# Optimization experiments

Measured on AMD Instinct MI355X. Metric: run time of the kernel, lower is better.

The kernel has to match this reference:

```python
import jax, jax.numpy as jnp
import numpy as np

B, T, C = 2, 2048, 1024
HS = 64              # head_size
H = C // HS          # 16 heads
DW, DA, DV, DG = 64, 64, 32, 160   # RWKV-7 LoRA dims for C=1024
FFN = 4 * C
GN_EPS = 64e-5       # ln_x GroupNorm eps from source


def _layernorm(h, w, b, eps=1e-5):
    mu = jnp.mean(h, axis=-1, keepdims=True)
    var = jnp.mean(jnp.square(h - mu), axis=-1, keepdims=True)
    return (h - mu) * jax.lax.rsqrt(var + eps) * w + b


def _time_shift_delta(h):
    # ZeroPad2d((0,0,1,-1))(h) - h : previous-token delta
    return jnp.pad(h, ((0, 0), (1, 0), (0, 0)))[:, :-1, :] - h


def _wkv7_scan(decay, r, k, v, a, b, S0):
    # all inputs [B,T,H,N]; state S [B,H,N_v,N_k]
    # S_t = S_{t-1} * diag(decay_t) + (S_{t-1} @ a_t) b_t^T + v_t k_t^T ; y_t = S_t @ r_t
    def step(S, inp):
        w_t, r_t, k_t, v_t, a_t, b_t = inp
        S = S * w_t[:, :, None, :]
        sa = jnp.einsum('bhij,bhj->bhi', S, a_t)
        S = S + sa[..., None] * b_t[:, :, None, :] + v_t[..., None] * k_t[:, :, None, :]
        y = jnp.einsum('bhij,bhj->bhi', S, r_t)
        return S, y
    seq = tuple(jnp.moveaxis(t, 1, 0) for t in (decay, r, k, v, a, b))
    S_last, y = jax.lax.scan(step, S0, seq)
    return jnp.moveaxis(y, 0, 1), S_last


def _block_forward(x, v_first, init_state, ln1_w, ln1_b, ln2_w, ln2_b,
                   x_r, x_w, x_k, x_v, x_a, x_g, w0, w1, w2, a0, a1, a2,
                   v0, v1, v2, g1, g2, k_k, k_a, r_k, W_r, W_k, W_v, W_o,
                   ln_x_w, ln_x_b, mix_k_ffn, W_key_ffn, W_val_ffn):
    # ---- time-mix (RWKV_Tmix_x070), layer_idx = 1 ----
    xn = _layernorm(x, ln1_w, ln1_b)
    xx = _time_shift_delta(xn)
    xr = xn + xx * x_r
    xw = xn + xx * x_w
    xk = xn + xx * x_k
    xv = xn + xx * x_v
    xa = xn + xx * x_a
    xg = xn + xx * x_g
    r = xr @ W_r.T
    w = -jax.nn.softplus(-(w0 + jnp.tanh(xw @ w1) @ w2)) - 0.5   # w <= -0.5
    k = xk @ W_k.T
    v = xv @ W_v.T
    v = v + (v_first - v) * jax.nn.sigmoid(v0 + (xv @ v1) @ v2)  # layer_idx > 0 path
    a = jax.nn.sigmoid(a0 + (xa @ a1) @ a2)
    g = jax.nn.sigmoid(xg @ g1) @ g2
    kk = (k * k_k).reshape(B, T, H, HS)
    kk = kk / jnp.maximum(jnp.linalg.norm(kk, axis=-1, keepdims=True), 1e-12)
    k = k * (1.0 + (a - 1.0) * k_a)
    r4 = r.reshape(B, T, H, HS)
    k4 = k.reshape(B, T, H, HS)
    v4 = v.reshape(B, T, H, HS)
    a4 = a.reshape(B, T, H, HS)
    decay = jnp.exp(w).reshape(B, T, H, HS)
    y, S_last = _wkv7_scan(decay, r4, k4, v4, -kk, kk * a4, init_state)
    # GroupNorm(H groups, eps=64e-5) over C, per (b,t)
    mu = jnp.mean(y, axis=-1, keepdims=True)
    var = jnp.mean(jnp.square(y - mu), axis=-1, keepdims=True)
    y = ((y - mu) * jax.lax.rsqrt(var + GN_EPS)).reshape(B, T, C) * ln_x_w + ln_x_b
    y = y + (jnp.sum(r4 * k4 * r_k, axis=-1, keepdims=True) * v4).reshape(B, T, C)
    x = x + (y * g) @ W_o.T
    # ---- channel-mix (RWKV_CMix_x070) ----
    xn2 = _layernorm(x, ln2_w, ln2_b)
    kf = xn2 + _time_shift_delta(xn2) * mix_k_ffn
    kf = jnp.square(jax.nn.relu(kf @ W_key_ffn.T))
    x = x + kf @ W_val_ffn.T
    return x, v_first


def setup_inputs():
    key = jax.random.key(0)
    ks = iter(jax.random.split(key, 40))
    def nrm(shape, s):
        return jax.random.normal(next(ks), shape, dtype=jnp.float32) * s
    def uni(shape, lo=0.0, hi=1.0):
        return jax.random.uniform(next(ks), shape, dtype=jnp.float32, minval=lo, maxval=hi)
    return {
        'x': nrm((B, T, C), 1.0),
        'v_first': nrm((B, T, C), 1.0),
        'init_state': jnp.zeros((B, H, HS, HS), jnp.float32),
        'ln1_w': jnp.ones((C,), jnp.float32), 'ln1_b': jnp.zeros((C,), jnp.float32),
        'ln2_w': jnp.ones((C,), jnp.float32), 'ln2_b': jnp.zeros((C,), jnp.float32),
        'x_r': uni((C,)), 'x_w': uni((C,)), 'x_k': uni((C,)),
        'x_v': uni((C,)), 'x_a': uni((C,)), 'x_g': uni((C,)),
        'w0': uni((C,), -6.5, -1.5),
        'w1': nrm((C, DW), 0.02), 'w2': nrm((DW, C), 0.02),
        'a0': jnp.zeros((C,), jnp.float32),
        'a1': nrm((C, DA), 0.02), 'a2': nrm((DA, C), 0.02),
        'v0': jnp.ones((C,), jnp.float32),
        'v1': nrm((C, DV), 0.02), 'v2': nrm((DV, C), 0.02),
        'g1': nrm((C, DG), 0.02), 'g2': nrm((DG, C), 0.02),
        'k_k': 0.85 * jnp.ones((C,), jnp.float32),
        'k_a': jnp.ones((C,), jnp.float32),
        'r_k': nrm((H, HS), 0.02),
        'W_r': nrm((C, C), 0.02), 'W_k': nrm((C, C), 0.02),
        'W_v': nrm((C, C), 0.02), 'W_o': nrm((C, C), 0.02),
        'ln_x_w': jnp.ones((C,), jnp.float32), 'ln_x_b': jnp.zeros((C,), jnp.float32),
        'mix_k_ffn': uni((C,)),
        'W_key_ffn': nrm((FFN, C), 0.02), 'W_val_ffn': nrm((C, FFN), 0.02),
    }


def reference(x, v_first, init_state, ln1_w, ln1_b, ln2_w, ln2_b,
              x_r, x_w, x_k, x_v, x_a, x_g, w0, w1, w2, a0, a1, a2,
              v0, v1, v2, g1, g2, k_k, k_a, r_k, W_r, W_k, W_v, W_o,
              ln_x_w, ln_x_b, mix_k_ffn, W_key_ffn, W_val_ffn):
    return _block_forward(x, v_first, init_state, ln1_w, ln1_b, ln2_w, ln2_b,
                          x_r, x_w, x_k, x_v, x_a, x_g, w0, w1, w2, a0, a1, a2,
                          v0, v1, v2, g1, g2, k_k, k_a, r_k, W_r, W_k, W_v, W_o,
                          ln_x_w, ln_x_b, mix_k_ffn, W_key_ffn, W_val_ffn)
```

## Files before the change

### kernel.cpp

```cpp
#include <hip/hip_runtime.h>
#include <math.h>

#define Bb 2
#define Tt 2048
#define Cc 1024
#define Hh 16
#define BT 4096
#define FFNd 4096
#define CH 16
#define CL 128
#define WU 32
#define BIGN 3456
#define BIGK 2048
#define LORAK 320
#define BIGW 4096

typedef __attribute__((ext_vector_type(8))) short bf16x8;
typedef __attribute__((ext_vector_type(4))) float f32x4;
typedef unsigned short u16;

__device__ __forceinline__ float sgm(float x){ return 1.0f/(1.0f+expf(-x)); }

template<int MAXM>
__device__ __forceinline__ float redgrp(float v){
  #pragma unroll
  for (int m=1; m<=MAXM; m<<=1) v += __shfl_xor(v, m, 64);
  return v;
}

template<int CTRL>
__device__ __forceinline__ float dppadd(float v){
  union { float f; int i; } u, r;
  u.f = v;
  r.i = __builtin_amdgcn_update_dpp(u.i, u.i, CTRL, 0xf, 0xf, true);
  return v + r.f;
}
__device__ __forceinline__ float red16(float v){
  v = dppadd<0xB1>(v);
  v = dppadd<0x4E>(v);
  v = dppadd<0x141>(v);
  v = dppadd<0x140>(v);
  return v;
}

__device__ __forceinline__ unsigned pack_bf16(float a, float b){
  unsigned ua = __builtin_bit_cast(unsigned, a);
  unsigned ub = __builtin_bit_cast(unsigned, b);
  ua = (ua + 0x7FFFu + ((ua>>16)&1u)) >> 16;
  ub = (ub + 0x7FFFu + ((ub>>16)&1u)) >> 16;
  return ua | (ub<<16);
}
__device__ __forceinline__ u16 bf16_1(float a){
  unsigned ua = __builtin_bit_cast(unsigned, a);
  return (u16)((ua + 0x7FFFu + ((ua>>16)&1u)) >> 16);
}

__device__ __forceinline__ void gload16(const void* g, void* l){
  __builtin_amdgcn_global_load_lds(
    (const __attribute__((address_space(1))) unsigned int*)g,
    (__attribute__((address_space(3))) unsigned int*)l, 16, 0, 0);
}

__global__ __launch_bounds__(256) void cvt_kernel(const float* __restrict__ in,
    u16* __restrict__ out) {
  size_t i = (size_t)blockIdx.x*256 + threadIdx.x;
  float4 a = ((const float4*)in)[2*i];
  float4 b = ((const float4*)in)[2*i+1];
  uint4 o = {pack_bf16(a.x,a.y), pack_bf16(a.z,a.w),
             pack_bf16(b.x,b.y), pack_bf16(b.z,b.w)};
  ((uint4*)out)[i] = o;
}

__global__ __launch_bounds__(256) void packW_kernel(const float* __restrict__ Wr,
    const float* __restrict__ Wk, const float* __restrict__ Wv,
    const float* __restrict__ xr, const float* __restrict__ xk,
    const float* __restrict__ xv, u16* __restrict__ out) {
  int which = blockIdx.y;
  const float* W   = which==0 ? Wr : (which==1 ? Wk : Wv);
  const float* mix = which==0 ? xr : (which==1 ? xk : xv);
  u16* o = out + (size_t)which*1024*BIGK;
  int n = blockIdx.x;
  int c0 = threadIdx.x*8;
  int ks = c0 & 1023;
  const float* src = W + (size_t)n*Cc + ks;
  float4 a = *(const float4*)src;
  float4 b = *(const float4*)(src+4);
  if (c0 >= 1024){
    float4 m0 = *(const float4*)(mix + ks);
    float4 m1 = *(const float4*)(mix + ks + 4);
    a.x*=m0.x; a.y*=m0.y; a.z*=m0.z; a.w*=m0.w;
    b.x*=m1.x; b.y*=m1.y; b.z*=m1.z; b.w*=m1.w;
  }
  uint4 ov = {pack_bf16(a.x,a.y), pack_bf16(a.z,a.w),
              pack_bf16(b.x,b.y), pack_bf16(b.z,b.w)};
  *(uint4*)(o + (size_t)n*BIGK + c0) = ov;
}

__global__ __launch_bounds__(256) void packL_kernel(const float* __restrict__ w1,
    const float* __restrict__ a1, const float* __restrict__ v1,
    const float* __restrict__ g1, const float* __restrict__ x_w,
    const float* __restrict__ x_a, const float* __restrict__ x_v,
    const float* __restrict__ x_g, u16* __restrict__ out) {
  int bid = blockIdx.x;
  const float* W1; const float* mix; int D, d, nbase;
  if (bid < 64)       { W1=w1; mix=x_w; D=64;  d=bid;     nbase=3072; }
  else if (bid < 128) { W1=a1; mix=x_a; D=64;  d=bid-64;  nbase=3136; }
  else if (bid < 160) { W1=v1; mix=x_v; D=32;  d=bid-128; nbase=3200; }
  else                { W1=g1; mix=x_g; D=160; d=bid-160; nbase=3232; }
  int k0 = threadIdx.x*8;
  float v[8];
  #pragma unroll
  for (int q=0;q<8;++q){
    int kk = k0+q;
    int ks = kk & 1023;
    float t = W1[(size_t)ks*D + d];
    if (kk >= 1024) t *= mix[ks];
    v[q] = t;
  }
  uint4 o = {pack_bf16(v[0],v[1]), pack_bf16(v[2],v[3]),
             pack_bf16(v[4],v[5]), pack_bf16(v[6],v[7])};
  *(uint4*)(out + (size_t)(nbase+d)*BIGK + k0) = o;
}

__global__ __launch_bounds__(320) void packW2_kernel(const float* __restrict__ w2,
    const float* __restrict__ a2, const float* __restrict__ v2,
    const float* __restrict__ g2, u16* __restrict__ out) {
  int n = blockIdx.x; int k = threadIdx.x;
  int which = n >> 10, col = n & 1023;
  float v = 0.f;
  if (which==0)      { if (k < 64)              v = w2[(size_t)k*Cc + col]; }
  else if (which==1) { if (k >= 64 && k < 128)  v = a2[(size_t)(k-64)*Cc + col]; }
  else if (which==2) { if (k >= 128 && k < 160) v = v2[(size_t)(k-128)*Cc + col]; }
  else               { if (k >= 160)            v = g2[(size_t)(k-160)*Cc + col]; }
  out[(size_t)n*LORAK + k] = bf16_1(v);
}

__global__ __launch_bounds__(320) void actcvt_kernel(const float* __restrict__ m,
    u16* __restrict__ loraAct) {
  int i = blockIdx.x; int cc = threadIdx.x;
  float v = m[(size_t)i*BIGN + 3072 + cc];
  if (cc < 64) v = tanhf(v);
  else if (cc >= 160) v = sgm(v);
  loraAct[(size_t)i*LORAK + cc] = bf16_1(v);
}

__global__ __launch_bounds__(256) void lnmix1_kernel(const float* __restrict__ x,
    const float* __restrict__ w, const float* __restrict__ b,
    u16* __restrict__ bigA) {
  int rowg = blockIdx.x; int t = rowg & (Tt-1);
  int tid = threadIdx.x;
  size_t off = (size_t)rowg*Cc + tid*4;
  float4 vc = *(const float4*)(x + off);
  float4 vp = {0.f,0.f,0.f,0.f};
  if (t) vp = *(const float4*)(x + off - Cc);
  float sc = vc.x+vc.y+vc.z+vc.w;
  float qc = vc.x*vc.x+vc.y*vc.y+vc.z*vc.z+vc.w*vc.w;
  float sp = vp.x+vp.y+vp.z+vp.w;
  float qp = vp.x*vp.x+vp.y*vp.y+vp.z*vp.z+vp.w*vp.w;
  sc = redgrp<32>(sc); qc = redgrp<32>(qc);
  sp = redgrp<32>(sp); qp = redgrp<32>(qp);
  __shared__ float rbuf[4][4];
  int lane = tid & 63, wv = tid >> 6;
  if (lane==0){ rbuf[wv][0]=sc; rbuf[wv][1]=qc; rbuf[wv][2]=sp; rbuf[wv][3]=qp; }
  __syncthreads();
  sc = rbuf[0][0]+rbuf[1][0]+rbuf[2][0]+rbuf[3][0];
  qc = rbuf[0][1]+rbuf[1][1]+rbuf[2][1]+rbuf[3][1];
  sp = rbuf[0][2]+rbuf[1][2]+rbuf[2][2]+rbuf[3][2];
  qp = rbuf[0][3]+rbuf[1][3]+rbuf[2][3]+rbuf[3][3];
  float muc = sc*(1.0f/Cc), mup = sp*(1.0f/Cc);
  float rnc = rsqrtf(qc*(1.0f/Cc) - muc*muc + 1e-5f);
  float rnp = rsqrtf(qp*(1.0f/Cc) - mup*mup + 1e-5f);
  float4 w4 = *(const float4*)(w + tid*4);
  float4 b4 = *(const float4*)(b + tid*4);
  float vcl[4]={vc.x,vc.y,vc.z,vc.w};
  float vpl[4]={vp.x,vp.y,vp.z,vp.w};
  float wl[4]={w4.x,w4.y,w4.z,w4.w};
  float bl[4]={b4.x,b4.y,b4.z,b4.w};
  float xnc[4], xx[4];
  #pragma unroll
  for (int q=0;q<4;++q){
    xnc[q] = (vcl[q]-muc)*rnc*wl[q] + bl[q];
    float xnp = t ? ((vpl[q]-mup)*rnp*wl[q] + bl[q]) : 0.0f;
    xx[q] = xnp - xnc[q];
  }
  size_t ab = (size_t)rowg*BIGK + tid*4;
  uint2 p0 = {pack_bf16(xnc[0],xnc[1]), pack_bf16(xnc[2],xnc[3])};
  uint2 p1 = {pack_bf16(xx[0],xx[1]),   pack_bf16(xx[2],xx[3])};
  *(uint2*)(bigA + ab) = p0;
  *(uint2*)(bigA + ab + 1024) = p1;
}

__global__ __launch_bounds__(256) void lnmix2_kernel(const float* __restrict__ x,
    const float* __restrict__ w, const float* __restrict__ b,
    const float* __restrict__ mixk, u16* __restrict__ outb) {
  int rowg = blockIdx.x; int t = rowg & (Tt-1);
  int tid = threadIdx.x;
  size_t off = (size_t)rowg*Cc + tid*4;
  float4 vc = *(const float4*)(x + off);
  float4 vp = {0.f,0.f,0.f,0.f};
  if (t) vp = *(const float4*)(x + off - Cc);
  float sc = vc.x+vc.y+vc.z+vc.w;
  float qc = vc.x*vc.x+vc.y*vc.y+vc.z*vc.z+vc.w*vc.w;
  float sp = vp.x+vp.y+vp.z+vp.w;
  float qp = vp.x*vp.x+vp.y*vp.y+vp.z*vp.z+vp.w*vp.w;
  sc = redgrp<32>(sc); qc = redgrp<32>(qc);
  sp = redgrp<32>(sp); qp = redgrp<32>(qp);
  __shared__ float rbuf[4][4];
  int lane = tid & 63, wv = tid >> 6;
  if (lane==0){ rbuf[wv][0]=sc; rbuf[wv][1]=qc; rbuf[wv][2]=sp; rbuf[wv][3]=qp; }
  __syncthreads();
  sc = rbuf[0][0]+rbuf[1][0]+rbuf[2][0]+rbuf[3][0];
  qc = rbuf[0][1]+rbuf[1][1]+rbuf[2][1]+rbuf[3][1];
  sp = rbuf[0][2]+rbuf[1][2]+rbuf[2][2]+rbuf[3][2];
  qp = rbuf[0][3]+rbuf[1][3]+rbuf[2][3]+rbuf[3][3];
  float muc = sc*(1.0f/Cc), mup = sp*(1.0f/Cc);
  float rnc = rsqrtf(qc*(1.0f/Cc) - muc*muc + 1e-5f);
  float rnp = rsqrtf(qp*(1.0f/Cc) - mup*mup + 1e-5f);
  float4 w4 = *(const float4*)(w + tid*4);
  float4 b4 = *(const float4*)(b + tid*4);
  float4 m = *(const float4*)(mixk + tid*4);
  float vcl[4]={vc.x,vc.y,vc.z,vc.w};
  float vpl[4]={vp.x,vp.y,vp.z,vp.w};
  float wl[4]={w4.x,w4.y,w4.z,w4.w};
  float bl[4]={b4.x,b4.y,b4.z,b4.w};
  float ml[4]={m.x,m.y,m.z,m.w};
  float o[4];
  #pragma unroll
  for (int q=0;q<4;++q){
    float xnc = (vcl[q]-muc)*rnc*wl[q] + bl[q];
    float xnp = t ? ((vpl[q]-mup)*rnp*wl[q] + bl[q]) : 0.0f;
    o[q] = xnc + (xnp - xnc)*ml[q];
  }
  uint2 p = {pack_bf16(o[0],o[1]), pack_bf16(o[2],o[3])};
  *(uint2*)(outb + off) = p;
}

template<int MODE>
__global__ __launch_bounds__(256) void gemm_bf16(const u16* __restrict__ A,
    const u16* __restrict__ W, void* __restrict__ outv,
    const float* __restrict__ res, int M, int N, int K) {
  __shared__ u16 As[2][128*64];
  __shared__ u16 Bs[2][128*64];
  int tid = threadIdx.x;
  int nwg = gridDim.x;
  int q8 = nwg >> 3;
  int id = (blockIdx.x & 7)*q8 + (blockIdx.x >> 3);
  int nbx = N >> 7;
  int bm = id / nbx, bn = id - bm*nbx;
  int wave = tid >> 6, lane = tid & 63;
  int wm = wave >> 1, wn = wave & 1;
  int srow = wave*32 + (lane>>3);
  int scol = (((lane&7) ^ ((lane>>3)&7)))*8;
  const u16* Ag = A + (size_t)(bm*128 + srow)*K + scol;
  const u16* Wg = W + (size_t)(bn*128 + srow)*K + scol;
  int nt = K >> 6;
  f32x4 acc[4][4];
  f32x4 zero = {0.f,0.f,0.f,0.f};
  #pragma unroll
  for (int i=0;i<4;++i)
    #pragma unroll
    for (int j=0;j<4;++j) acc[i][j] = zero;

  #define STAGE(buf, t) { \
    const u16* Ag2 = Ag + (size_t)(t)*64; \
    const u16* Wg2 = Wg + (size_t)(t)*64; \
    _Pragma("unroll") \
    for (int i_=0;i_<4;++i_){ \
      gload16(Ag2 + (size_t)i_*8*K, &As[buf][(wave*32+i_*8)*64]); \
      gload16(Wg2 + (size_t)i_*8*K, &Bs[buf][(wave*32+i_*8)*64]); \
    } }

  STAGE(0, 0);
  int lrow = lane & 15, lk8 = lane >> 4;
  int r7 = lrow & 7;
  for (int t = 0; t < nt; ++t) {
    int cur = t & 1;
    if (t+1 < nt) {
      STAGE(cur^1, t+1);
      asm volatile("s_waitcnt vmcnt(8)\n\ts_barrier" ::: "memory");
    } else {
      asm volatile("s_waitcnt vmcnt(0)\n\ts_barrier" ::: "memory");
    }
    #pragma unroll
    for (int kk2 = 0; kk2 < 2; ++kk2) {
      int sl = ((kk2*4 + lk8) ^ r7) * 8;
      bf16x8 af[4], bfr[4];
      #pragma unroll
      for (int i=0;i<4;++i)
        af[i] = *(const bf16x8*)&As[cur][(wm*64 + i*16 + lrow)*64 + sl];
      #pragma unroll
      for (int j=0;j<4;++j)
        bfr[j] = *(const bf16x8*)&Bs[cur][(wn*64 + j*16 + lrow)*64 + sl];
      #pragma unroll
      for (int i=0;i<4;++i)
        #pragma unroll
        for (int j=0;j<4;++j)
          acc[i][j] = __builtin_amdgcn_mfma_f32_16x16x32_bf16(af[i], bfr[j], acc[i][j], 0, 0, 0);
    }
    asm volatile("s_barrier" ::: "memory");
  }
  #undef STAGE
  float* outf = (float*)outv;
  u16* outb = (u16*)outv;
  int crow4 = (lane>>4)*4, ccol = lane & 15;
  #pragma unroll
  for (int i=0;i<4;++i){
    #pragma unroll
    for (int j=0;j<4;++j){
      int gr = bm*128 + wm*64 + i*16 + crow4;
      int gc = bn*128 + wn*64 + j*16 + ccol;
      #pragma unroll
      for (int q=0;q<4;++q){
        float v = acc[i][j][q];
        size_t o = (size_t)(gr+q)*N + gc;
        if (MODE==1) { v += res[o]; outf[o] = v; }
        else if (MODE==2) { v = fmaxf(v, 0.f); outb[o] = bf16_1(v*v); }
        else outf[o] = v;
      }
    }
  }
}

__global__ __launch_bounds__(256) void prep_kernel(
    const float* __restrict__ kraw, const float* __restrict__ dw,
    const float* __restrict__ da, const float* __restrict__ dv,
    const float* __restrict__ vraw, const float* __restrict__ vfirst,
    const float* __restrict__ w0, const float* __restrict__ a0,
    const float* __restrict__ v0, const float* __restrict__ k_k,
    const float* __restrict__ k_a,
    float* __restrict__ decay, float* __restrict__ kfin, float* __restrict__ vfin,
    float* __restrict__ Ak, float* __restrict__ Bk) {
  int row = blockIdx.x; int tid = threadIdx.x; int c = tid*4;
  size_t off = (size_t)row*Cc + c;
  size_t offw = (size_t)row*BIGN + c;
  size_t offd = (size_t)row*BIGW + c;
  float4 kr = *(const float4*)(kraw+offw);
  float4 vr = *(const float4*)(vraw+offw);
  float4 w4 = *(const float4*)(dw+offd);
  float4 A4 = *(const float4*)(da+offd);
  float4 V4 = *(const float4*)(dv+offd);
  float4 vf = *(const float4*)(vfirst+off);
  float4 w04 = *(const float4*)(w0+c);
  float4 a04 = *(const float4*)(a0+c);
  float4 v04 = *(const float4*)(v0+c);
  float4 kk4 = *(const float4*)(k_k+c);
  float4 ka4 = *(const float4*)(k_a+c);
  float krl[4]={kr.x,kr.y,kr.z,kr.w};
  float dwl[4]={w4.x,w4.y,w4.z,w4.w};
  float dal[4]={A4.x,A4.y,A4.z,A4.w};
  float dvl[4]={V4.x,V4.y,V4.z,V4.w};
  float vrl[4]={vr.x,vr.y,vr.z,vr.w};
  float vfl[4]={vf.x,vf.y,vf.z,vf.w};
  float w0l[4]={w04.x,w04.y,w04.z,w04.w};
  float a0l[4]={a04.x,a04.y,a04.z,a04.w};
  float v0l[4]={v04.x,v04.y,v04.z,v04.w};
  float kkl[4]={kk4.x,kk4.y,kk4.z,kk4.w};
  float kal[4]={ka4.x,ka4.y,ka4.z,ka4.w};
  float av[4], dec[4], vv[4], kp[4], kf[4];
  float ss = 0.f;
  #pragma unroll
  for (int q=0;q<4;++q){
    av[q] = sgm(a0l[q] + dal[q]);
    dec[q] = 0.60653065971263342f * sgm(w0l[q] + dwl[q]);
    float sv = sgm(v0l[q] + dvl[q]);
    vv[q] = vrl[q] + (vfl[q]-vrl[q])*sv;
    kp[q] = krl[q]*kkl[q];
    ss += kp[q]*kp[q];
    kf[q] = krl[q]*(1.0f + (av[q]-1.0f)*kal[q]);
  }
  ss = redgrp<8>(ss);
  float inv = 1.0f / fmaxf(sqrtf(ss), 1e-12f);
  float4 o;
  o.x=dec[0];o.y=dec[1];o.z=dec[2];o.w=dec[3];  *(float4*)(decay+off)=o;
  o.x=kf[0]; o.y=kf[1]; o.z=kf[2]; o.w=kf[3];   *(float4*)(kfin+off)=o;
  o.x=vv[0]; o.y=vv[1]; o.z=vv[2]; o.w=vv[3];   *(float4*)(vfin+off)=o;
  o.x=-kp[0]*inv; o.y=-kp[1]*inv; o.z=-kp[2]*inv; o.w=-kp[3]*inv; *(float4*)(Ak+off)=o;
  o.x=kp[0]*inv*av[0]; o.y=kp[1]*inv*av[1]; o.z=kp[2]*inv*av[2]; o.w=kp[3]*inv*av[3];
  *(float4*)(Bk+off)=o;
}

__global__ __launch_bounds__(512) void wkv_kernel(
    const float* __restrict__ decay, const float* __restrict__ Ak,
    const float* __restrict__ Bk, const float* __restrict__ kfin,
    const float* __restrict__ r_, const float* __restrict__ vfin,
    const float* __restrict__ S0, float* __restrict__ y) {
  __shared__ float lds[2][6][CH][64];
  int bid = blockIdx.x;
  int bh = bid & 31, c = bid >> 5;
  int bb = bh >> 4, h = bh & 15;
  int tid = threadIdx.x;
  int wave = tid >> 6, lane = tid & 63;
  int rg = tid >> 4;
  int bj = tid & 15, j0 = bj*4;
  int r0 = rg, r1 = rg + 32;
  float Sa_[4] = {0.f,0.f,0.f,0.f};
  float Sb_[4] = {0.f,0.f,0.f,0.f};
  if (c == 0) {
    float4 t0 = *(const float4*)(S0 + (size_t)bh*4096 + r0*64 + j0);
    float4 t1 = *(const float4*)(S0 + (size_t)bh*4096 + r1*64 + j0);
    Sa_[0]=t0.x; Sa_[1]=t0.y; Sa_[2]=t0.z; Sa_[3]=t0.w;
    Sb_[0]=t1.x; Sb_[1]=t1.y; Sb_[2]=t1.z; Sb_[3]=t1.w;
  }
  size_t seqb = (size_t)bb*Tt;
  int t0g = (c==0) ? 0 : (c*CL - WU);
  int NPH = (c==0) ? (CL/CH) : ((CL+WU)/CH);
  int phE = (c==0) ? 0 : (WU/CH);
  int lhi = lane >> 4, llo4 = (lane & 15)*4;

  #define WST1(buf, stepb, arr, base, ldv) { \
    const float* gp_ = (base) + (size_t)(seqb + (size_t)(stepb) + lhi)*(ldv) + h*64 + llo4; \
    _Pragma("unroll") \
    for (int p_=0; p_<4; ++p_) \
      gload16(gp_ + (size_t)p_*4*(ldv), &lds[buf][arr][p_*4][0]); }
  #define WSTAGE(buf, stepb) { \
    if (wave==0)      { WST1(buf, stepb, 0, decay, Cc) } \
    else if (wave==1) { WST1(buf, stepb, 1, Ak, Cc) } \
    else if (wave==2) { WST1(buf, stepb, 2, Bk, Cc) } \
    else if (wave==3) { WST1(buf, stepb, 3, kfin, Cc) } \
    else if (wave==4) { WST1(buf, stepb, 4, r_, BIGN) } \
    else if (wave==5) { WST1(buf, stepb, 5, vfin, Cc) } }

  WSTAGE(0, t0g);
  for (int ph = 0; ph < NPH; ++ph) {
    int cur = ph & 1;
    if (ph+1 < NPH) {
      WSTAGE(cur^1, t0g + (ph+1)*CH);
      asm volatile("s_waitcnt vmcnt(4)\n\ts_barrier" ::: "memory");
    } else {
      asm volatile("s_waitcnt vmcnt(0)\n\ts_barrier" ::: "memory");
    }
    bool emit = (ph >= phE);
    const float* L0 = &lds[cur][0][0][0];
    #pragma unroll
    for (int s = 0; s < CH; ++s) {
      const float* bp = L0 + s*64;
      float4 d4 = *(const float4*)(bp + 0*CH*64 + j0);
      float4 a4 = *(const float4*)(bp + 1*CH*64 + j0);
      float4 b4 = *(const float4*)(bp + 2*CH*64 + j0);
      float4 k4 = *(const float4*)(bp + 3*CH*64 + j0);
      float4 r4 = *(const float4*)(bp + 4*CH*64 + j0);
      float v0 = bp[5*CH*64 + r0];
      float v1 = bp[5*CH*64 + r1];
      Sa_[0]*=d4.x; Sa_[1]*=d4.y; Sa_[2]*=d4.z; Sa_[3]*=d4.w;
      Sb_[0]*=d4.x; Sb_[1]*=d4.y; Sb_[2]*=d4.z; Sb_[3]*=d4.w;
      float sa0 = fmaf(Sa_[0],a4.x, Sa_[1]*a4.y) + fmaf(Sa_[2],a4.z, Sa_[3]*a4.w);
      float sa1 = fmaf(Sb_[0],a4.x, Sb_[1]*a4.y) + fmaf(Sb_[2],a4.z, Sb_[3]*a4.w);
      sa0 = red16(sa0);
      sa1 = red16(sa1);
      Sa_[0]=fmaf(v0,k4.x,Sa_[0]); Sa_[1]=fmaf(v0,k4.y,Sa_[1]);
      Sa_[2]=fmaf(v0,k4.z,Sa_[2]); Sa_[3]=fmaf(v0,k4.w,Sa_[3]);
      Sa_[0]=fmaf(sa0,b4.x,Sa_[0]); Sa_[1]=fmaf(sa0,b4.y,Sa_[1]);
      Sa_[2]=fmaf(sa0,b4.z,Sa_[2]); Sa_[3]=fmaf(sa0,b4.w,Sa_[3]);
      Sb_[0]=fmaf(v1,k4.x,Sb_[0]); Sb_[1]=fmaf(v1,k4.y,Sb_[1]);
      Sb_[2]=fmaf(v1,k4.z,Sb_[2]); Sb_[3]=fmaf(v1,k4.w,Sb_[3]);
      Sb_[0]=fmaf(sa1,b4.x,Sb_[0]); Sb_[1]=fmaf(sa1,b4.y,Sb_[1]);
      Sb_[2]=fmaf(sa1,b4.z,Sb_[2]); Sb_[3]=fmaf(sa1,b4.w,Sb_[3]);
      if (emit) {
        float y0 = fmaf(Sa_[0],r4.x, Sa_[1]*r4.y) + fmaf(Sa_[2],r4.z, Sa_[3]*r4.w);
        float y1 = fmaf(Sb_[0],r4.x, Sb_[1]*r4.y) + fmaf(Sb_[2],r4.z, Sb_[3]*r4.w);
        y0 = red16(y0);
        y1 = red16(y1);
        if (bj == 0) {
          size_t yo = (seqb + (size_t)t0g + ph*CH + s)*Cc + h*64;
          y[yo + r0] = y0;
          y[yo + r1] = y1;
        }
      }
    }
    asm volatile("s_barrier" ::: "memory");
  }
  #undef WSTAGE
  #undef WST1
}

__global__ __launch_bounds__(256) void gn_kernel(
    const float* __restrict__ y, const float* __restrict__ r_,
    const float* __restrict__ kfin, const float* __restrict__ vfin,
    const float* __restrict__ g_, const float* __restrict__ lnxw,
    const float* __restrict__ lnxb, const float* __restrict__ r_k,
    u16* __restrict__ Ao) {
  int row = blockIdx.x; int tid = threadIdx.x; int c = tid*4;
  size_t off = (size_t)row*Cc + c;
  float4 y4 = *(const float4*)(y+off);
  float s = y4.x+y4.y+y4.z+y4.w;
  float q = y4.x*y4.x+y4.y*y4.y+y4.z*y4.z+y4.w*y4.w;
  s = redgrp<8>(s); q = redgrp<8>(q);
  float mu = s*(1.0f/64.0f);
  float var = q*(1.0f/64.0f) - mu*mu;
  float rn = rsqrtf(var + 64e-5f);
  float4 rr = *(const float4*)(r_ + (size_t)row*BIGN + c);
  float4 kk = *(const float4*)(kfin+off);
  float4 vv = *(const float4*)(vfin+off);
  float4 gg = *(const float4*)(g_ + (size_t)row*BIGW + c);
  int h = tid >> 4; int hs = (tid & 15)*4;
  float4 rk = *(const float4*)(r_k + h*64 + hs);
  float dp = rr.x*kk.x*rk.x + rr.y*kk.y*rk.y + rr.z*kk.z*rk.z + rr.w*kk.w*rk.w;
  dp = redgrp<8>(dp);
  float4 w4 = *(const float4*)(lnxw+c);
  float4 b4 = *(const float4*)(lnxb+c);
  float o0 = (((y4.x-mu)*rn)*w4.x + b4.x + dp*vv.x) * gg.x;
  float o1 = (((y4.y-mu)*rn)*w4.y + b4.y + dp*vv.y) * gg.y;
  float o2 = (((y4.z-mu)*rn)*w4.z + b4.z + dp*vv.z) * gg.z;
  float o3 = (((y4.w-mu)*rn)*w4.w + b4.w + dp*vv.w) * gg.w;
  uint2 p = {pack_bf16(o0,o1), pack_bf16(o2,o3)};
  *(uint2*)(Ao + off) = p;
}

__global__ __launch_bounds__(256) void copy_kernel(const float* __restrict__ src,
                                                   float* __restrict__ dst) {
  size_t i = ((size_t)blockIdx.x*256 + threadIdx.x)*4;
  *(float4*)(dst+i) = *(const float4*)(src+i);
}

extern "C" void kernel_launch(void* const* d_in, const int* in_sizes, int n_in,
                              void* d_out, int out_size, void* d_ws, size_t ws_size,
                              hipStream_t stream) {
  const float* x      = (const float*)d_in[0];
  const float* vfirst = (const float*)d_in[1];
  const float* S0     = (const float*)d_in[2];
  const float* ln1w   = (const float*)d_in[3];
  const float* ln1b   = (const float*)d_in[4];
  const float* ln2w   = (const float*)d_in[5];
  const float* ln2b   = (const float*)d_in[6];
  const float* x_r    = (const float*)d_in[7];
  const float* x_w    = (const float*)d_in[8];
  const float* x_k    = (const float*)d_in[9];
  const float* x_v    = (const float*)d_in[10];
  const float* x_a    = (const float*)d_in[11];
  const float* x_g    = (const float*)d_in[12];
  const float* w0     = (const float*)d_in[13];
  const float* w1     = (const float*)d_in[14];
  const float* w2     = (const float*)d_in[15];
  const float* a0     = (const float*)d_in[16];
  const float* a1     = (const float*)d_in[17];
  const float* a2     = (const float*)d_in[18];
  const float* v0     = (const float*)d_in[19];
  const float* v1     = (const float*)d_in[20];
  const float* v2     = (const float*)d_in[21];
  const float* g1     = (const float*)d_in[22];
  const float* g2     = (const float*)d_in[23];
  const float* k_k    = (const float*)d_in[24];
  const float* k_a    = (const float*)d_in[25];
  const float* r_k    = (const float*)d_in[26];
  const float* W_r    = (const float*)d_in[27];
  const float* W_k    = (const float*)d_in[28];
  const float* W_v    = (const float*)d_in[29];
  const float* W_o    = (const float*)d_in[30];
  const float* lnxw   = (const float*)d_in[31];
  const float* lnxb   = (const float*)d_in[32];
  const float* mixk   = (const float*)d_in[33];
  const float* Wkey   = (const float*)d_in[34];
  const float* Wval   = (const float*)d_in[35];
  float* out = (float*)d_out;
  float* ws  = (float*)d_ws;
  const size_t U = (size_t)BT * Cc;
  float* u[14];
  for (int i=0;i<14;++i) u[i] = ws + i*U;

  u16* bigA   = (u16*)u[0];
  u16* BigB   = (u16*)u[1];
  float* bigOut = u[2];
  float* dwdavg = u[6];
  u16* W2blk  = (u16*)u[10];
  u16* loraAct= (u16*)u[11];
  float* Bk   = u[0];
  float* y_   = u[1];
  u16* gnb    = (u16*)u[10];
  u16* Wob    = (u16*)u[13];
  float* xo   = u[0];
  u16* Wkeyb  = (u16*)u[6];
  u16* cmb    = (u16*)u[7];
  u16* Wvalb  = (u16*)u[8];
  u16* midb   = (u16*)u[2];

  dim3 b256(256);
  packW_kernel<<<dim3(Cc,3), b256, 0, stream>>>(W_r, W_k, W_v, x_r, x_k, x_v, BigB);
  packL_kernel<<<320, b256, 0, stream>>>(w1, a1, v1, g1, x_w, x_a, x_v, x_g, BigB);
  packW2_kernel<<<BIGW, dim3(320), 0, stream>>>(w2, a2, v2, g2, W2blk);
  lnmix1_kernel<<<BT, b256, 0, stream>>>(x, ln1w, ln1b, bigA);
  gemm_bf16<0><<<(BT/128)*(BIGN/128), b256, 0, stream>>>(bigA, BigB, bigOut, nullptr, BT, BIGN, BIGK);
  actcvt_kernel<<<BT, dim3(320), 0, stream>>>(bigOut, loraAct);
  gemm_bf16<0><<<(BT/128)*(BIGW/128), b256, 0, stream>>>(loraAct, W2blk, dwdavg, nullptr, BT, BIGW, LORAK);
  prep_kernel<<<BT, b256, 0, stream>>>(bigOut+1024, dwdavg, dwdavg+1024, dwdavg+2048,
      bigOut+2048, vfirst, w0, a0, v0, k_k, k_a, u[10], u[11], u[12], u[13], Bk);
  wkv_kernel<<<32*(Tt/CL), dim3(512), 0, stream>>>(u[10], u[13], Bk, u[11], bigOut, u[12], S0, y_);
  cvt_kernel<<<Cc*Cc/2048, b256, 0, stream>>>(W_o, Wob);
  gn_kernel<<<BT, b256, 0, stream>>>(y_, bigOut, u[11], u[12], dwdavg+3072, lnxw, lnxb, r_k, gnb);
  gemm_bf16<1><<<(BT/128)*(Cc/128), b256, 0, stream>>>(gnb, Wob, xo, x, BT, Cc, Cc);
  lnmix2_kernel<<<BT, b256, 0, stream>>>(xo, ln2w, ln2b, mixk, cmb);
  cvt_kernel<<<FFNd*Cc/2048, b256, 0, stream>>>(Wkey, Wkeyb);
  gemm_bf16<2><<<(BT/128)*(FFNd/128), b256, 0, stream>>>(cmb, Wkeyb, midb, nullptr, BT, FFNd, Cc);
  cvt_kernel<<<Cc*FFNd/2048, b256, 0, stream>>>(Wval, Wvalb);
  gemm_bf16<1><<<(BT/128)*(Cc/128), b256, 0, stream>>>(midb, Wvalb, out, xo, BT, Cc, FFNd);
  copy_kernel<<<BT*Cc/1024, b256, 0, stream>>>(vfirst, out + (size_t)BT*Cc);
}
```

Before: 411.6 us.

## Add 256x256-tile GEMM and fuse LoRA activation into big GEMM epilogue

Introduces a 512-thread GEMM with 256x256 output tiles for the fused projection GEMM, the LoRA second-stage GEMM and the FFN key GEMM, raising data reuse per workgroup. The tanh/sigmoid conversion of LoRA activations is moved into the projection GEMM's epilogue, removing the separate actcvt kernel and its round trip. BIGN is padded to a multiple of 256, which adds wasted columns of compute. The larger tiles also cut the number of workgroups, which risks under-filling the GPU, and use more LDS and registers.

```diff
diff --git a/kernel.cpp b/kernel.cpp
--- a/kernel.cpp
+++ b/kernel.cpp
@@ -10,7 +10,7 @@
 #define CH 16
 #define CL 128
 #define WU 32
-#define BIGN 3456
+#define BIGN 3584
 #define BIGK 2048
 #define LORAK 320
 #define BIGW 4096
@@ -133,15 +133,6 @@
   else if (which==2) { if (k >= 128 && k < 160) v = v2[(size_t)(k-128)*Cc + col]; }
   else               { if (k >= 160)            v = g2[(size_t)(k-160)*Cc + col]; }
   out[(size_t)n*LORAK + k] = bf16_1(v);
-}
-
-__global__ __launch_bounds__(320) void actcvt_kernel(const float* __restrict__ m,
-    u16* __restrict__ loraAct) {
-  int i = blockIdx.x; int cc = threadIdx.x;
-  float v = m[(size_t)i*BIGN + 3072 + cc];
-  if (cc < 64) v = tanhf(v);
-  else if (cc >= 160) v = sgm(v);
-  loraAct[(size_t)i*LORAK + cc] = bf16_1(v);
 }
 
 __global__ __launch_bounds__(256) void lnmix1_kernel(const float* __restrict__ x,
@@ -233,6 +224,101 @@
   }
   uint2 p = {pack_bf16(o[0],o[1]), pack_bf16(o[2],o[3])};
   *(uint2*)(outb + off) = p;
+}
+
+template<int MODE>
+__global__ __launch_bounds__(512) void gemm256(const u16* __restrict__ A,
+    const u16* __restrict__ W, void* __restrict__ outv,
+    u16* __restrict__ lora, int M, int N, int K) {
+  __shared__ u16 As[2][256*64];
+  __shared__ u16 Bs[2][256*64];
+  int tid = threadIdx.x;
+  int nwg = gridDim.x;
+  int q8 = nwg >> 3;
+  int id = (blockIdx.x & 7)*q8 + (blockIdx.x >> 3);
+  int nbx = N >> 8;
+  int bm = id / nbx, bn = id - bm*nbx;
+  int wave = tid >> 6, lane = tid & 63;
+  int wm = wave >> 2, wn = wave & 3;
+  int sr8 = lane >> 3;
+  int schunk = (lane & 7) ^ sr8;
+  const u16* Ag = A + (size_t)(bm*256 + wave*32 + sr8)*K + schunk*8;
+  const u16* Wg = W + (size_t)(bn*256 + wave*32 + sr8)*K + schunk*8;
+  int nt = K >> 6;
+  f32x4 acc[8][4];
+  f32x4 zero = {0.f,0.f,0.f,0.f};
+  #pragma unroll
+  for (int i=0;i<8;++i)
+    #pragma unroll
+    for (int j=0;j<4;++j) acc[i][j] = zero;
+
+  #define ST(buf, t) { \
+    const u16* Ag2 = Ag + (size_t)(t)*64; \
+    const u16* Wg2 = Wg + (size_t)(t)*64; \
+    _Pragma("unroll") \
+    for (int l_=0;l_<4;++l_){ \
+      gload16(Ag2 + (size_t)l_*8*K, &As[buf][wave*2048 + l_*512]); \
+      gload16(Wg2 + (size_t)l_*8*K, &Bs[buf][wave*2048 + l_*512]); \
+    } }
+
+  ST(0, 0);
+  int lrow = lane & 15, lk8 = lane >> 4;
+  int r7 = lrow & 7;
+  for (int t = 0; t < nt; ++t) {
+    int cur = t & 1;
+    if (t+1 < nt) {
+      ST(cur^1, t+1);
+      asm volatile("s_waitcnt vmcnt(8)\n\ts_barrier" ::: "memory");
+    } else {
+      asm volatile("s_waitcnt vmcnt(0)\n\ts_barrier" ::: "memory");
+    }
+    #pragma unroll
+    for (int kk2 = 0; kk2 < 2; ++kk2) {
+      int sl = ((kk2*4 + lk8) ^ r7) * 8;
+      bf16x8 af[8], bfr[4];
+      #pragma unroll
+      for (int i=0;i<8;++i)
+        af[i] = *(const bf16x8*)&As[cur][(wm*128 + i*16 + lrow)*64 + sl];
+      #pragma unroll
+      for (int j=0;j<4;++j)
+        bfr[j] = *(const bf16x8*)&Bs[cur][(wn*64 + j*16 + lrow)*64 + sl];
+      #pragma unroll
+      for (int i=0;i<8;++i)
+        #pragma unroll
+        for (int j=0;j<4;++j)
+          acc[i][j] = __builtin_amdgcn_mfma_f32_16x16x32_bf16(af[i], bfr[j], acc[i][j], 0, 0, 0);
+    }
+    asm volatile("s_barrier" ::: "memory");
+  }
+  #undef ST
+  float* outf = (float*)outv;
+  u16* outb = (u16*)outv;
+  int crow4 = (lane>>4)*4, ccol = lane & 15;
+  #pragma unroll
+  for (int i=0;i<8;++i){
+    #pragma unroll
+    for (int j=0;j<4;++j){
+      int gr = bm*256 + wm*128 + i*16 + crow4;
+      int gc = bn*256 + wn*64 + j*16 + ccol;
+      #pragma unroll
+      for (int q=0;q<4;++q){
+        float v = acc[i][j][q];
+        size_t o = (size_t)(gr+q)*N + gc;
+        if (MODE==2) { v = fmaxf(v, 0.f); outb[o] = bf16_1(v*v); }
+        else if (MODE==3) {
+          if (gc < 3072) outf[o] = v;
+          else if (gc < 3392) {
+            int cc = gc - 3072;
+            float a = v;
+            if (cc < 64) a = tanhf(a);
+            else if (cc >= 160) a = sgm(a);
+            lora[(size_t)(gr+q)*LORAK + cc] = bf16_1(a);
+          }
+        }
+        else outf[o] = v;
+      }
+    }
+  }
 }
 
 template<int MODE>
@@ -578,9 +664,8 @@
   packL_kernel<<<320, b256, 0, stream>>>(w1, a1, v1, g1, x_w, x_a, x_v, x_g, BigB);
   packW2_kernel<<<BIGW, dim3(320), 0, stream>>>(w2, a2, v2, g2, W2blk);
   lnmix1_kernel<<<BT, b256, 0, stream>>>(x, ln1w, ln1b, bigA);
-  gemm_bf16<0><<<(BT/128)*(BIGN/128), b256, 0, stream>>>(bigA, BigB, bigOut, nullptr, BT, BIGN, BIGK);
-  actcvt_kernel<<<BT, dim3(320), 0, stream>>>(bigOut, loraAct);
-  gemm_bf16<0><<<(BT/128)*(BIGW/128), b256, 0, stream>>>(loraAct, W2blk, dwdavg, nullptr, BT, BIGW, LORAK);
+  gemm256<3><<<(BT/256)*(BIGN/256), dim3(512), 0, stream>>>(bigA, BigB, bigOut, loraAct, BT, BIGN, BIGK);
+  gemm256<0><<<(BT/256)*(BIGW/256), dim3(512), 0, stream>>>(loraAct, W2blk, dwdavg, nullptr, BT, BIGW, LORAK);
   prep_kernel<<<BT, b256, 0, stream>>>(bigOut+1024, dwdavg, dwdavg+1024, dwdavg+2048,
       bigOut+2048, vfirst, w0, a0, v0, k_k, k_a, u[10], u[11], u[12], u[13], Bk);
   wkv_kernel<<<32*(Tt/CL), dim3(512), 0, stream>>>(u[10], u[13], Bk, u[11], bigOut, u[12], S0, y_);
@@ -589,7 +674,7 @@
   gemm_bf16<1><<<(BT/128)*(Cc/128), b256, 0, stream>>>(gnb, Wob, xo, x, BT, Cc, Cc);
   lnmix2_kernel<<<BT, b256, 0, stream>>>(xo, ln2w, ln2b, mixk, cmb);
   cvt_kernel<<<FFNd*Cc/2048, b256, 0, stream>>>(Wkey, Wkeyb);
-  gemm_bf16<2><<<(BT/128)*(FFNd/128), b256, 0, stream>>>(cmb, Wkeyb, midb, nullptr, BT, FFNd, Cc);
+  gemm256<2><<<(BT/256)*(FFNd/256), dim3(512), 0, stream>>>(cmb, Wkeyb, midb, nullptr, BT, FFNd, Cc);
   cvt_kernel<<<Cc*FFNd/2048, b256, 0, stream>>>(Wval, Wvalb);
   gemm_bf16<1><<<(BT/128)*(Cc/128), b256, 0, stream>>>(midb, Wvalb, out, xo, BT, Cc, FFNd);
   copy_kernel<<<BT*Cc/1024, b256, 0, stream>>>(vfirst, out + (size_t)BT*Cc);
```

Result: slower. 424.1 us (+3.0%).

## Fuse LoRA activation into big GEMM epilogue and halve WKV threads per head

Applied to the files above, without the earlier changes.

The tanh/sigmoid LoRA activation and bf16 conversion now run in a new epilogue mode of the large projection GEMM. This removes the separate actcvt kernel and the fp32 write and re-read of the LoRA columns. The WKV scan block drops from 512 to 256 threads, with each thread holding four state rows instead of two. The load waves now each stage two arrays, with the wait counts adjusted to match. This cuts the number of cross-lane reductions and barriers per state row, but each thread does more serial work in the latency-bound scan.

```diff
diff --git a/kernel.cpp b/kernel.cpp
--- a/kernel.cpp
+++ b/kernel.cpp
@@ -133,15 +133,6 @@
   else if (which==2) { if (k >= 128 && k < 160) v = v2[(size_t)(k-128)*Cc + col]; }
   else               { if (k >= 160)            v = g2[(size_t)(k-160)*Cc + col]; }
   out[(size_t)n*LORAK + k] = bf16_1(v);
-}
-
-__global__ __launch_bounds__(320) void actcvt_kernel(const float* __restrict__ m,
-    u16* __restrict__ loraAct) {
-  int i = blockIdx.x; int cc = threadIdx.x;
-  float v = m[(size_t)i*BIGN + 3072 + cc];
-  if (cc < 64) v = tanhf(v);
-  else if (cc >= 160) v = sgm(v);
-  loraAct[(size_t)i*LORAK + cc] = bf16_1(v);
 }
 
 __global__ __launch_bounds__(256) void lnmix1_kernel(const float* __restrict__ x,
@@ -238,7 +229,8 @@
 template<int MODE>
 __global__ __launch_bounds__(256) void gemm_bf16(const u16* __restrict__ A,
     const u16* __restrict__ W, void* __restrict__ outv,
-    const float* __restrict__ res, int M, int N, int K) {
+    const float* __restrict__ res, u16* __restrict__ lora,
+    int M, int N, int K) {
   __shared__ u16 As[2][128*64];
   __shared__ u16 Bs[2][128*64];
   int tid = threadIdx.x;
@@ -315,6 +307,16 @@
         size_t o = (size_t)(gr+q)*N + gc;
         if (MODE==1) { v += res[o]; outf[o] = v; }
         else if (MODE==2) { v = fmaxf(v, 0.f); outb[o] = bf16_1(v*v); }
+        else if (MODE==3) {
+          if (gc < 3072) outf[o] = v;
+          else if (gc < 3392) {
+            int cc = gc - 3072;
+            float a = v;
+            if (cc < 64) a = tanhf(a);
+            else if (cc >= 160) a = sgm(a);
+            lora[(size_t)(gr+q)*LORAK + cc] = bf16_1(a);
+          }
+        }
         else outf[o] = v;
       }
     }
@@ -379,7 +381,7 @@
   *(float4*)(Bk+off)=o;
 }
 
-__global__ __launch_bounds__(512) void wkv_kernel(
+__global__ __launch_bounds__(256) void wkv_kernel(
     const float* __restrict__ decay, const float* __restrict__ Ak,
     const float* __restrict__ Bk, const float* __restrict__ kfin,
     const float* __restrict__ r_, const float* __restrict__ vfin,
@@ -392,14 +394,18 @@
   int wave = tid >> 6, lane = tid & 63;
   int rg = tid >> 4;
   int bj = tid & 15, j0 = bj*4;
-  int r0 = rg, r1 = rg + 32;
-  float Sa_[4] = {0.f,0.f,0.f,0.f};
-  float Sb_[4] = {0.f,0.f,0.f,0.f};
+  float S0r[4], S1r[4], S2r[4], S3r[4];
+  #pragma unroll
+  for (int q=0;q<4;++q){ S0r[q]=0.f; S1r[q]=0.f; S2r[q]=0.f; S3r[q]=0.f; }
   if (c == 0) {
-    float4 t0 = *(const float4*)(S0 + (size_t)bh*4096 + r0*64 + j0);
-    float4 t1 = *(const float4*)(S0 + (size_t)bh*4096 + r1*64 + j0);
-    Sa_[0]=t0.x; Sa_[1]=t0.y; Sa_[2]=t0.z; Sa_[3]=t0.w;
-    Sb_[0]=t1.x; Sb_[1]=t1.y; Sb_[2]=t1.z; Sb_[3]=t1.w;
+    float4 t0 = *(const float4*)(S0 + (size_t)bh*4096 + (rg+ 0)*64 + j0);
+    float4 t1 = *(const float4*)(S0 + (size_t)bh*4096 + (rg+16)*64 + j0);
+    float4 t2 = *(const float4*)(S0 + (size_t)bh*4096 + (rg+32)*64 + j0);
+    float4 t3 = *(const float4*)(S0 + (size_t)bh*4096 + (rg+48)*64 + j0);
+    S0r[0]=t0.x; S0r[1]=t0.y; S0r[2]=t0.z; S0r[3]=t0.w;
+    S1r[0]=t1.x; S1r[1]=t1.y; S1r[2]=t1.z; S1r[3]=t1.w;
+    S2r[0]=t2.x; S2r[1]=t2.y; S2r[2]=t2.z; S2r[3]=t2.w;
+    S3r[0]=t3.x; S3r[1]=t3.y; S3r[2]=t3.z; S3r[3]=t3.w;
   }
   size_t seqb = (size_t)bb*Tt;
   int t0g = (c==0) ? 0 : (c*CL - WU);
@@ -413,19 +419,19 @@
     for (int p_=0; p_<4; ++p_) \
       gload16(gp_ + (size_t)p_*4*(ldv), &lds[buf][arr][p_*4][0]); }
   #define WSTAGE(buf, stepb) { \
-    if (wave==0)      { WST1(buf, stepb, 0, decay, Cc) } \
-    else if (wave==1) { WST1(buf, stepb, 1, Ak, Cc) } \
-    else if (wave==2) { WST1(buf, stepb, 2, Bk, Cc) } \
-    else if (wave==3) { WST1(buf, stepb, 3, kfin, Cc) } \
-    else if (wave==4) { WST1(buf, stepb, 4, r_, BIGN) } \
-    else if (wave==5) { WST1(buf, stepb, 5, vfin, Cc) } }
+    if (wave==0)      { WST1(buf, stepb, 0, decay, Cc) WST1(buf, stepb, 1, Ak, Cc) } \
+    else if (wave==1) { WST1(buf, stepb, 2, Bk, Cc)   WST1(buf, stepb, 3, kfin, Cc) } \
+    else if (wave==2) { WST1(buf, stepb, 4, r_, BIGN) } \
+    else              { WST1(buf, stepb, 5, vfin, Cc) } }
 
   WSTAGE(0, t0g);
   for (int ph = 0; ph < NPH; ++ph) {
     int cur = ph & 1;
     if (ph+1 < NPH) {
       WSTAGE(cur^1, t0g + (ph+1)*CH);
-      asm volatile("s_waitcnt vmcnt(4)\n\ts_barrier" ::: "memory");
+      if (wave < 2) asm volatile("s_waitcnt vmcnt(8)" ::: "memory");
+      else          asm volatile("s_waitcnt vmcnt(4)" ::: "memory");
+      asm volatile("s_barrier" ::: "memory");
     } else {
       asm volatile("s_waitcnt vmcnt(0)\n\ts_barrier" ::: "memory");
     }
@@ -439,31 +445,47 @@
       float4 b4 = *(const float4*)(bp + 2*CH*64 + j0);
       float4 k4 = *(const float4*)(bp + 3*CH*64 + j0);
       float4 r4 = *(const float4*)(bp + 4*CH*64 + j0);
-      float v0 = bp[5*CH*64 + r0];
-      float v1 = bp[5*CH*64 + r1];
-      Sa_[0]*=d4.x; Sa_[1]*=d4.y; Sa_[2]*=d4.z; Sa_[3]*=d4.w;
-      Sb_[0]*=d4.x; Sb_[1]*=d4.y; Sb_[2]*=d4.z; Sb_[3]*=d4.w;
-      float sa0 = fmaf(Sa_[0],a4.x, Sa_[1]*a4.y) + fmaf(Sa_[2],a4.z, Sa_[3]*a4.w);
-      float sa1 = fmaf(Sb_[0],a4.x, Sb_[1]*a4.y) + fmaf(Sb_[2],a4.z, Sb_[3]*a4.w);
-      sa0 = red16(sa0);
-      sa1 = red16(sa1);
-      Sa_[0]=fmaf(v0,k4.x,Sa_[0]); Sa_[1]=fmaf(v0,k4.y,Sa_[1]);
-      Sa_[2]=fmaf(v0,k4.z,Sa_[2]); Sa_[3]=fmaf(v0,k4.w,Sa_[3]);
-      Sa_[0]=fmaf(sa0,b4.x,Sa_[0]); Sa_[1]=fmaf(sa0,b4.y,Sa_[1]);
-      Sa_[2]=fmaf(sa0,b4.z,Sa_[2]); Sa_[3]=fmaf(sa0,b4.w,Sa_[3]);
-      Sb_[0]=fmaf(v1,k4.x,Sb_[0]); Sb_[1]=fmaf(v1,k4.y,Sb_[1]);
-      Sb_[2]=fmaf(v1,k4.z,Sb_[2]); Sb_[3]=fmaf(v1,k4.w,Sb_[3]);
-      Sb_[0]=fmaf(sa1,b4.x,Sb_[0]); Sb_[1]=fmaf(sa1,b4.y,Sb_[1]);
-      Sb_[2]=fmaf(sa1,b4.z,Sb_[2]); Sb_[3]=fmaf(sa1,b4.w,Sb_[3]);
+      float v0 = bp[5*CH*64 + rg];
+      float v1 = bp[5*CH*64 + rg+16];
+      float v2 = bp[5*CH*64 + rg+32];
+      float v3 = bp[5*CH*64 + rg+48];
+      S0r[0]*=d4.x; S0r[1]*=d4.y; S0r[2]*=d4.z; S0r[3]*=d4.w;
+      S1r[0]*=d4.x; S1r[1]*=d4.y; S1r[2]*=d4.z; S1r[3]*=d4.w;
+      S2r[0]*=d4.x; S2r[1]*=d4.y; S2r[2]*=d4.z; S2r[3]*=d4.w;
+      S3r[0]*=d4.x; S3r[1]*=d4.y; S3r[2]*=d4.z; S3r[3]*=d4.w;
+      float sa0 = fmaf(S0r[0],a4.x, S0r[1]*a4.y) + fmaf(S0r[2],a4.z, S0r[3]*a4.w);
+      float sa1 = fmaf(S1r[0],a4.x, S1r[1]*a4.y) + fmaf(S1r[2],a4.z, S1r[3]*a4.w);
+      float sa2 = fmaf(S2r[0],a4.x, S2r[1]*a4.y) + fmaf(S2r[2],a4.z, S2r[3]*a4.w);
+      float sa3 = fmaf(S3r[0],a4.x, S3r[1]*a4.y) + fmaf(S3r[2],a4.z, S3r[3]*a4.w);
+      sa0 = red16(sa0); sa1 = red16(sa1); sa2 = red16(sa2); sa3 = red16(sa3);
+      S0r[0]=fmaf(v0,k4.x,S0r[0]); S0r[1]=fmaf(v0,k4.y,S0r[1]);
+      S0r[2]=fmaf(v0,k4.z,S0r[2]); S0r[3]=fmaf(v0,k4.w,S0r[3]);
+      S0r[0]=fmaf(sa0,b4.x,S0r[0]); S0r[1]=fmaf(sa0,b4.y,S0r[1]);
+      S0r[2]=fmaf(sa0,b4.z,S0r[2]); S0r[3]=fmaf(sa0,b4.w,S0r[3]);
+      S1r[0]=fmaf(v1,k4.x,S1r[0]); S1r[1]=fmaf(v1,k4.y,S1r[1]);
+      S1r[2]=fmaf(v1,k4.z,S1r[2]); S1r[3]=fmaf(v1,k4.w,S1r[3]);
+      S1r[0]=fmaf(sa1,b4.x,S1r[0]); S1r[1]=fmaf(sa1,b4.y,S1r[1]);
+      S1r[2]=fmaf(sa1,b4.z,S1r[2]); S1r[3]=fmaf(sa1,b4.w,S1r[3]);
+      S2r[0]=fmaf(v2,k4.x,S2r[0]); S2r[1]=fmaf(v2,k4.y,S2r[1]);
+      S2r[2]=fmaf(v2,k4.z,S2r[2]); S2r[3]=fmaf(v2,k4.w,S2r[3]);
+      S2r[0]=fmaf(sa2,b4.x,S2r[0]); S2r[1]=fmaf(sa2,b4.y,S2r[1]);
+      S2r[2]=fmaf(sa2,b4.z,S2r[2]); S2r[3]=fmaf(sa2,b4.w,S2r[3]);
+      S3r[0]=fmaf(v3,k4.x,S3r[0]); S3r[1]=fmaf(v3,k4.y,S3r[1]);
+      S3r[2]=fmaf(v3,k4.z,S3r[2]); S3r[3]=fmaf(v3,k4.w,S3r[3]);
+      S3r[0]=fmaf(sa3,b4.x,S3r[0]); S3r[1]=fmaf(sa3,b4.y,S3r[1]);
+      S3r[2]=fmaf(sa3,b4.z,S3r[2]); S3r[3]=fmaf(sa3,b4.w,S3r[3]);
       if (emit) {
-        float y0 = fmaf(Sa_[0],r4.x, Sa_[1]*r4.y) + fmaf(Sa_[2],r4.z, Sa_[3]*r4.w);
-        float y1 = fmaf(Sb_[0],r4.x, Sb_[1]*r4.y) + fmaf(Sb_[2],r4.z, Sb_[3]*r4.w);
-        y0 = red16(y0);
-        y1 = red16(y1);
+        float y0 = fmaf(S0r[0],r4.x, S0r[1]*r4.y) + fmaf(S0r[2],r4.z, S0r[3]*r4.w);
+        float y1 = fmaf(S1r[0],r4.x, S1r[1]*r4.y) + fmaf(S1r[2],r4.z, S1r[3]*r4.w);
+        float y2 = fmaf(S2r[0],r4.x, S2r[1]*r4.y) + fmaf(S2r[2],r4.z, S2r[3]*r4.w);
+        float y3 = fmaf(S3r[0],r4.x, S3r[1]*r4.y) + fmaf(S3r[2],r4.z, S3r[3]*r4.w);
+        y0 = red16(y0); y1 = red16(y1); y2 = red16(y2); y3 = red16(y3);
         if (bj == 0) {
           size_t yo = (seqb + (size_t)t0g + ph*CH + s)*Cc + h*64;
-          y[yo + r0] = y0;
-          y[yo + r1] = y1;
+          y[yo + rg     ] = y0;
+          y[yo + rg + 16] = y1;
+          y[yo + rg + 32] = y2;
+          y[yo + rg + 48] = y3;
         }
       }
     }
@@ -578,19 +600,18 @@
   packL_kernel<<<320, b256, 0, stream>>>(w1, a1, v1, g1, x_w, x_a, x_v, x_g, BigB);
   packW2_kernel<<<BIGW, dim3(320), 0, stream>>>(w2, a2, v2, g2, W2blk);
   lnmix1_kernel<<<BT, b256, 0, stream>>>(x, ln1w, ln1b, bigA);
-  gemm_bf16<0><<<(BT/128)*(BIGN/128), b256, 0, stream>>>(bigA, BigB, bigOut, nullptr, BT, BIGN, BIGK);
-  actcvt_kernel<<<BT, dim3(320), 0, stream>>>(bigOut, loraAct);
-  gemm_bf16<0><<<(BT/128)*(BIGW/128), b256, 0, stream>>>(loraAct, W2blk, dwdavg, nullptr, BT, BIGW, LORAK);
+  gemm_bf16<3><<<(BT/128)*(BIGN/128), b256, 0, stream>>>(bigA, BigB, bigOut, nullptr, loraAct, BT, BIGN, BIGK);
+  gemm_bf16<0><<<(BT/128)*(BIGW/128), b256, 0, stream>>>(loraAct, W2blk, dwdavg, nullptr, nullptr, BT, BIGW, LORAK);
   prep_kernel<<<BT, b256, 0, stream>>>(bigOut+1024, dwdavg, dwdavg+1024, dwdavg+2048,
       bigOut+2048, vfirst, w0, a0, v0, k_k, k_a, u[10], u[11], u[12], u[13], Bk);
-  wkv_kernel<<<32*(Tt/CL), dim3(512), 0, stream>>>(u[10], u[13], Bk, u[11], bigOut, u[12], S0, y_);
+  wkv_kernel<<<32*(Tt/CL), b256, 0, stream>>>(u[10], u[13], Bk, u[11], bigOut, u[12], S0, y_);
   cvt_kernel<<<Cc*Cc/2048, b256, 0, stream>>>(W_o, Wob);
   gn_kernel<<<BT, b256, 0, stream>>>(y_, bigOut, u[11], u[12], dwdavg+3072, lnxw, lnxb, r_k, gnb);
-  gemm_bf16<1><<<(BT/128)*(Cc/128), b256, 0, stream>>>(gnb, Wob, xo, x, BT, Cc, Cc);
+  gemm_bf16<1><<<(BT/128)*(Cc/128), b256, 0, stream>>>(gnb, Wob, xo, x, nullptr, BT, Cc, Cc);
   lnmix2_kernel<<<BT, b256, 0, stream>>>(xo, ln2w, ln2b, mixk, cmb);
   cvt_kernel<<<FFNd*Cc/2048, b256, 0, stream>>>(Wkey, Wkeyb);
-  gemm_bf16<2><<<(BT/128)*(FFNd/128), b256, 0, stream>>>(cmb, Wkeyb, midb, nullptr, BT, FFNd, Cc);
+  gemm_bf16<2><<<(BT/128)*(FFNd/128), b256, 0, stream>>>(cmb, Wkeyb, midb, nullptr, nullptr, BT, FFNd, Cc);
   cvt_kernel<<<Cc*FFNd/2048, b256, 0, stream>>>(Wval, Wvalb);
-  gemm_bf16<1><<<(BT/128)*(Cc/128), b256, 0, stream>>>(midb, Wvalb, out, xo, BT, Cc, FFNd);
+  gemm_bf16<1><<<(BT/128)*(Cc/128), b256, 0, stream>>>(midb, Wvalb, out, xo, nullptr, BT, Cc, FFNd);
   copy_kernel<<<BT*Cc/1024, b256, 0, stream>>>(vfirst, out + (size_t)BT*Cc);
 }
```

New measurement: 439.8 us. +6.8%, slower.
